# Kernel tuning notes

Measured on AMD Instinct MI355X. Metric: run time of the kernel, lower is better.

The kernel has to match this reference:

```python
import jax, jax.numpy as jnp
import numpy as np
from jax import lax

X_SIZE, Z_SIZE, H, GC, PD = 256, 64, 64, 16, 2
B, K, T = 256, 16, 50
LOG_SIG_MIN, LOG_SIG_MAX, LOG_P_MAX = -10.0, 10.0, 50.0
ZX = X_SIZE + Z_SIZE
LSTM_IN = ZX + PD


def setup_inputs() -> dict:
    key = jax.random.key(0)
    ks = jax.random.split(key, 24)
    s = lambda fan_in: 1.0 / np.sqrt(fan_in)
    u = lambda k, shape, sc: jax.random.uniform(k, shape, jnp.float32, -sc, sc)
    inp = {
        'x': jax.random.normal(ks[0], (B, X_SIZE), jnp.float32),
        'z_stacked': jax.random.normal(ks[1], (K, B, Z_SIZE), jnp.float32),
        'input_seqs': jax.random.normal(ks[2], (B, 8, 2, 2, 6), jnp.float32),
        'pred_seqs': jax.random.normal(ks[3], (B, T, 2, 2, 6), jnp.float32),
        # initial_h / initial_c linears: ZX -> H
        'Wh0': u(ks[4], (H, ZX), s(ZX)), 'bh0': u(ks[5], (H,), s(ZX)),
        'Wc0': u(ks[6], (H, ZX), s(ZX)), 'bc0': u(ks[7], (H,), s(ZX)),
        # LSTMCell: gates order i,f,g,o
        'Wih': u(ks[8], (4 * H, LSTM_IN), s(H)), 'Whh': u(ks[9], (4 * H, H), s(H)),
        'bih': u(ks[10], (4 * H,), s(H)), 'bhh': u(ks[11], (4 * H,), s(H)),
        # GMM parameter heads: H -> GC / GC*PD
        'Wpi': u(ks[12], (GC, H), s(H)), 'bpi': u(ks[13], (GC,), s(H)),
        'Wmu': u(ks[14], (GC * PD, H), s(H)), 'bmu': u(ks[15], (GC * PD,), s(H)),
        'Wls': u(ks[16], (GC * PD, H), s(H)), 'bls': u(ks[17], (GC * PD,), s(H)),
        'Wcorr': u(ks[18], (GC, H), s(H)), 'bcorr': u(ks[19], (GC,), s(H)),
        'n_z_samples': K,
    }
    return inp


def _gmm2d_log_prob(log_pis, mus, log_sigmas, corrs, value):
    # log_pis/corrs: [K,B,T,GC]; mus/log_sigmas: [K,B,T,GC*PD]; value: [B,T,PD]
    ls = jnp.clip(log_sigmas, LOG_SIG_MIN, LOG_SIG_MAX).reshape(K, B, T, GC, PD)
    mu = mus.reshape(K, B, T, GC, PD)
    dx = value[None, :, :, None, :] - mu                      # [K,B,T,GC,PD]
    zscore = dx * jnp.exp(-ls)                                # dx / sigma
    one_m_rho2 = 1.0 - corrs ** 2
    quad = (zscore[..., 0] ** 2 + zscore[..., 1] ** 2
            - 2.0 * corrs * zscore[..., 0] * zscore[..., 1])
    comp = (-jnp.log(2.0 * jnp.pi) - ls.sum(-1)
            - 0.5 * jnp.log(one_m_rho2) - 0.5 * quad / one_m_rho2)
    log_pi_n = jax.nn.log_softmax(log_pis, axis=-1)
    log_p_t = jax.nn.logsumexp(log_pi_n + comp, axis=-1)      # [K,B,T]
    return jnp.minimum(log_p_t, LOG_P_MAX)


def reference(x, z_stacked, input_seqs, pred_seqs,
              Wh0, bh0, Wc0, bc0, Wih, Whh, bih, bhh,
              Wpi, bpi, Wmu, bmu, Wls, bls, Wcorr, bcorr, n_z_samples):
    tgt_future = pred_seqs[:, :, 1, 1, 2:4]                   # [B,T,2]
    tgt_present = input_seqs[:, -1, 1, 1, 2:4]                # [B,2]
    z = z_stacked.reshape(-1, z_stacked.shape[-1])            # [K*B, z]
    zx = jnp.concatenate([z, jnp.tile(x, (n_z_samples, 1))], axis=1)  # [N, ZX]
    N = zx.shape[0]
    h0 = zx @ Wh0.T + bh0
    c0 = zx @ Wc0.T + bc0
    decode_inputs = jnp.concatenate([tgt_present[:, None, :], tgt_future[:, :T - 1, :]], axis=1)  # [B,T,2]
    inputs = jnp.concatenate([
        jnp.broadcast_to(zx[:, None, :], (N, T, ZX)),
        jnp.tile(decode_inputs, (n_z_samples, 1, 1))], axis=2)  # [N,T,ZX+2]

    def step(carry, xt):
        h, c = carry
        gates = xt @ Wih.T + bih + h @ Whh.T + bhh
        i, f, g, o = jnp.split(gates, 4, axis=-1)
        c = jax.nn.sigmoid(f) * c + jax.nn.sigmoid(i) * jnp.tanh(g)
        h = jax.nn.sigmoid(o) * jnp.tanh(c)
        return (h, c), h

    _, hs = lax.scan(step, (h0, c0), jnp.swapaxes(inputs, 0, 1))  # [T,N,H]
    hs = jnp.swapaxes(hs, 0, 1)                                   # [N,T,H]

    log_pis = (hs @ Wpi.T + bpi).reshape(K, B, T, GC)
    mus = (hs @ Wmu.T + bmu).reshape(K, B, T, GC * PD)
    log_sigmas = (hs @ Wls.T + bls).reshape(K, B, T, GC * PD)
    corrs = jnp.tanh(hs @ Wcorr.T + bcorr).reshape(K, B, T, GC)

    log_p_yt_xz = _gmm2d_log_prob(log_pis, mus, log_sigmas, corrs, tgt_future)
    return log_p_yt_xz.sum(axis=2)                                # [K,B]
```

## Files before the change

kernel.cpp:

```cpp
#include <hip/hip_runtime.h>


#define T_ 50
#define SPB 16
#define ZXS 324
#define HFS 72
#define GLS 256
#define PLS 100

typedef __attribute__((ext_vector_type(8))) short short8;
typedef __attribute__((ext_vector_type(4))) float f32x4;

#define MFMA(a, b, c) __builtin_amdgcn_mfma_f32_16x16x32_bf16(a, b, c, 0, 0, 0)

__device__ __forceinline__ float sigf(float x)  { return 1.0f / (1.0f + __expf(-x)); }
__device__ __forceinline__ float tanh_(float x) { return 1.0f - 2.0f / (__expf(2.0f * x) + 1.0f); }

__device__ __forceinline__ void splitf(float f, unsigned short& hi, unsigned short& lo) {
    unsigned b = __float_as_uint(f);
    hi = (unsigned short)(b >> 16);
    float fh = __uint_as_float(b & 0xffff0000u);
    lo = (unsigned short)(__float_as_uint(f - fh) >> 16);
}

__device__ __forceinline__ void pack8(const float* p, short8& hi, short8& lo) {
    #pragma unroll
    for (int e = 0; e < 8; ++e) {
        unsigned short h, l;
        splitf(p[e], h, l);
        hi[e] = (short)h; lo[e] = (short)l;
    }
}

__launch_bounds__(512, 2)
__global__ void decoder_kernel(
    const float* __restrict__ x,       const float* __restrict__ z,
    const float* __restrict__ inp_seqs,const float* __restrict__ pred_seqs,
    const float* __restrict__ Wh0,     const float* __restrict__ bh0,
    const float* __restrict__ Wc0,     const float* __restrict__ bc0,
    const float* __restrict__ Wih,     const float* __restrict__ Whh,
    const float* __restrict__ bih,     const float* __restrict__ bhh,
    const float* __restrict__ Wpi,     const float* __restrict__ bpi,
    const float* __restrict__ Wmu,     const float* __restrict__ bmu,
    const float* __restrict__ Wls,     const float* __restrict__ bls,
    const float* __restrict__ Wcorr,   const float* __restrict__ bcorr,
    float* __restrict__ out)
{
    __shared__ __align__(16) float smem[9504];
    float* ZXL = smem;
    float* GL  = smem;
    float* PL  = smem + 4096;
    float* C0X = smem + 5696;
    unsigned short* HFhi = (unsigned short*)(smem + 6720);
    unsigned short* HFlo = (unsigned short*)(smem + 7296);
    float* FUT = smem + 7872;
    float* PRS = smem + 9472;

    const int j = threadIdx.x;
    const int w = j >> 6;
    const int l = j & 63;
    const int g = l >> 4;
    const int c = l & 15;
    const int blk = blockIdx.x;

    for (int e = j; e < SPB*320; e += 512) {
        int s = e / 320, k = e - s*320;
        int n = blk*SPB + s; int kk = n >> 8; int b = n & 255;
        ZXL[s*ZXS + k] = (k < 64) ? z[(kk*256 + b)*64 + k] : x[b*256 + (k - 64)];
    }
    for (int e = j; e < T_*SPB; e += 512) {
        int t = e >> 4, s = e & 15;
        int b = (blk*SPB + s) & 255;
        float2 v = *reinterpret_cast<const float2*>(pred_seqs + b*1200 + t*24 + 20);
        FUT[t*32 + s*2] = v.x; FUT[t*32 + s*2 + 1] = v.y;
    }
    if (j < SPB) {
        int b = (blk*SPB + j) & 255;
        float2 v = *reinterpret_cast<const float2*>(inp_seqs + b*192 + 188);
        PRS[j*2] = v.x; PRS[j*2 + 1] = v.y;
    }
    __syncthreads();

    const int gate0 = w*32 + c;
    const int gate1 = w*32 + 16 + c;
    const int colB  = w*16 + c;

    f32x4 gc0, gc1, accB;
    {
        float bA0 = bih[gate0] + bhh[gate0];
        float bA1 = bih[gate1] + bhh[gate1];
        float bB  = (w < 4) ? bh0[colB] : bc0[colB - 64];
        gc0 = (f32x4){bA0, bA0, bA0, bA0};
        gc1 = (f32x4){bA1, bA1, bA1, bA1};
        accB = (f32x4){bB, bB, bB, bB};
    }
    const float* rowA0 = Wih + gate0*322;
    const float* rowA1 = Wih + gate1*322;
    const float* rowB  = (w < 4) ? (Wh0 + colB*320) : (Wc0 + (colB - 64)*320);

    for (int ks = 0; ks < 10; ++ks) {
        int k0 = ks*32 + g*8;
        short8 ahi, alo, b0h, b0l, b1h, b1l, bbh, bbl;
        pack8(&ZXL[c*ZXS + k0], ahi, alo);
        pack8(rowA0 + k0, b0h, b0l);
        pack8(rowA1 + k0, b1h, b1l);
        pack8(rowB  + k0, bbh, bbl);
        gc0  = MFMA(ahi, b0h, gc0);  gc0  = MFMA(ahi, b0l, gc0);  gc0  = MFMA(alo, b0h, gc0);
        gc1  = MFMA(ahi, b1h, gc1);  gc1  = MFMA(ahi, b1l, gc1);  gc1  = MFMA(alo, b1h, gc1);
        accB = MFMA(ahi, bbh, accB); accB = MFMA(ahi, bbl, accB); accB = MFMA(alo, bbh, accB);
    }

    if (w < 4) {
        #pragma unroll
        for (int r = 0; r < 4; ++r) {
            int s = g*4 + r;
            unsigned short hh, ll; splitf(accB[r], hh, ll);
            HFhi[s*HFS + colB] = hh; HFlo[s*HFS + colB] = ll;
        }
    } else {
        #pragma unroll
        for (int r = 0; r < 4; ++r) C0X[(g*4 + r)*64 + (colB - 64)] = accB[r];
    }

    const float wd00 = rowA0[320], wd01 = rowA0[321];
    const float wd10 = rowA1[320], wd11 = rowA1[321];
    short8 w1h00, w1l00, w1h01, w1l01, w1h10, w1l10, w1h11, w1l11;
    pack8(Whh + gate0*64 +      g*8, w1h00, w1l00);
    pack8(Whh + gate0*64 + 32 + g*8, w1h01, w1l01);
    pack8(Whh + gate1*64 +      g*8, w1h10, w1l10);
    pack8(Whh + gate1*64 + 32 + g*8, w1h11, w1l11);

    short8 b3h0, b3l0, b3h1, b3l1;
    float bias3;
    {
        int r3 = (w < 6) ? (w*16 + c) : 0;
        const float* prow; float bb;
        if (r3 < 16)      { prow = Wpi   + r3*64;       bb = bpi[r3]; }
        else if (r3 < 48) { prow = Wmu   + (r3-16)*64;  bb = bmu[r3-16]; }
        else if (r3 < 80) { prow = Wls   + (r3-48)*64;  bb = bls[r3-48]; }
        else              { prow = Wcorr + (r3-80)*64;  bb = bcorr[r3-80]; }
        bias3 = bb;
        pack8(prow +      g*8, b3h0, b3l0);
        pack8(prow + 32 + g*8, b3h1, b3l1);
    }

    __syncthreads();

    const int u2 = j & 63, sg2 = j >> 6;
    float cst0 = C0X[(2*sg2 + 0)*64 + u2];
    float cst1 = C0X[(2*sg2 + 1)*64 + u2];

    const int s3 = j >> 4, g3 = j & 15;
    float sum = 0.0f;

    for (int t = 0; t < T_; ++t) {
        {
            const float* dptr = (t == 0) ? PRS : &FUT[(t-1)*32];
            f32x4 a0, a1;
            #pragma unroll
            for (int r = 0; r < 4; ++r) {
                float2 dv = *reinterpret_cast<const float2*>(dptr + (g*4 + r)*2);
                a0[r] = gc0[r] + dv.x*wd00 + dv.y*wd01;
                a1[r] = gc1[r] + dv.x*wd10 + dv.y*wd11;
            }
            short8 ah0 = *reinterpret_cast<const short8*>(HFhi + c*HFS +      g*8);
            short8 al0 = *reinterpret_cast<const short8*>(HFlo + c*HFS +      g*8);
            short8 ah1 = *reinterpret_cast<const short8*>(HFhi + c*HFS + 32 + g*8);
            short8 al1 = *reinterpret_cast<const short8*>(HFlo + c*HFS + 32 + g*8);
            a0 = MFMA(ah0, w1h00, a0); a0 = MFMA(ah0, w1l00, a0); a0 = MFMA(al0, w1h00, a0);
            a0 = MFMA(ah1, w1h01, a0); a0 = MFMA(ah1, w1l01, a0); a0 = MFMA(al1, w1h01, a0);
            a1 = MFMA(ah0, w1h10, a1); a1 = MFMA(ah0, w1l10, a1); a1 = MFMA(al0, w1h10, a1);
            a1 = MFMA(ah1, w1h11, a1); a1 = MFMA(ah1, w1l11, a1); a1 = MFMA(al1, w1h11, a1);
            #pragma unroll
            for (int r = 0; r < 4; ++r) {
                GL[(g*4 + r)*GLS + gate0] = a0[r];
                GL[(g*4 + r)*GLS + gate1] = a1[r];
            }
        }
        __syncthreads();

        {
            #pragma unroll
            for (int i = 0; i < 2; ++i) {
                int s = 2*sg2 + i;
                float gi = GL[s*GLS + u2];
                float gf = GL[s*GLS + 64  + u2];
                float gg = GL[s*GLS + 128 + u2];
                float go = GL[s*GLS + 192 + u2];
                float cp = (i == 0) ? cst0 : cst1;
                float cc = sigf(gf)*cp + sigf(gi)*tanh_(gg);
                if (i == 0) cst0 = cc; else cst1 = cc;
                float hh = sigf(go)*tanh_(cc);
                unsigned short uh, ul; splitf(hh, uh, ul);
                HFhi[s*HFS + u2] = uh; HFlo[s*HFS + u2] = ul;
            }
        }
        __syncthreads();

        if (w < 6) {
            short8 ah0 = *reinterpret_cast<const short8*>(HFhi + c*HFS +      g*8);
            short8 al0 = *reinterpret_cast<const short8*>(HFlo + c*HFS +      g*8);
            short8 ah1 = *reinterpret_cast<const short8*>(HFhi + c*HFS + 32 + g*8);
            short8 al1 = *reinterpret_cast<const short8*>(HFlo + c*HFS + 32 + g*8);
            f32x4 p = (f32x4){bias3, bias3, bias3, bias3};
            p = MFMA(ah0, b3h0, p); p = MFMA(ah0, b3l0, p); p = MFMA(al0, b3h0, p);
            p = MFMA(ah1, b3h1, p); p = MFMA(ah1, b3l1, p); p = MFMA(al1, b3h1, p);
            #pragma unroll
            for (int r = 0; r < 4; ++r) PL[(g*4 + r)*PLS + w*16 + c] = p[r];
        }
        __syncthreads();

        if (j < 256) {
            const float* pls = PL + s3*PLS;
            float a_pi = pls[g3];
            float a_m0 = pls[16 + 2*g3], a_m1 = pls[17 + 2*g3];
            float l0   = pls[48 + 2*g3], l1   = pls[49 + 2*g3];
            float a_co = pls[80 + g3];
            float v0 = FUT[t*32 + s3*2], v1 = FUT[t*32 + s3*2 + 1];
            l0 = fminf(fmaxf(l0, -10.0f), 10.0f);
            l1 = fminf(fmaxf(l1, -10.0f), 10.0f);
            float z0 = (v0 - a_m0) * __expf(-l0);
            float z1 = (v1 - a_m1) * __expf(-l1);
            float ct = tanh_(a_co);
            float omr = 1.0f - ct*ct;
            float quad = z0*z0 + z1*z1 - 2.0f*ct*z0*z1;
            float comp = -1.8378770664093453f - (l0 + l1) - 0.5f*__logf(omr) - 0.5f*quad/omr;
            float a = a_pi + comp;
            float m1v = a, m2v = a_pi;
            #pragma unroll
            for (int off = 1; off < 16; off <<= 1) {
                m1v = fmaxf(m1v, __shfl_xor(m1v, off));
                m2v = fmaxf(m2v, __shfl_xor(m2v, off));
            }
            float e1 = __expf(a - m1v), e2 = __expf(a_pi - m2v);
            #pragma unroll
            for (int off = 1; off < 16; off <<= 1) {
                e1 += __shfl_xor(e1, off);
                e2 += __shfl_xor(e2, off);
            }
            float logp = (m1v + __logf(e1)) - (m2v + __logf(e2));
            sum += fminf(logp, 50.0f);
        }
    }

    if (j < 256 && g3 == 0) out[blk*SPB + s3] = sum;
}

extern "C" void kernel_launch(void* const* d_in, const int* in_sizes, int n_in,
                              void* d_out, int out_size, void* d_ws, size_t ws_size,
                              hipStream_t stream) {
    const float* x     = (const float*)d_in[0];
    const float* z     = (const float*)d_in[1];
    const float* iseq  = (const float*)d_in[2];
    const float* pseq  = (const float*)d_in[3];
    const float* Wh0   = (const float*)d_in[4];
    const float* bh0   = (const float*)d_in[5];
    const float* Wc0   = (const float*)d_in[6];
    const float* bc0   = (const float*)d_in[7];
    const float* Wih   = (const float*)d_in[8];
    const float* Whh   = (const float*)d_in[9];
    const float* bih   = (const float*)d_in[10];
    const float* bhh   = (const float*)d_in[11];
    const float* Wpi   = (const float*)d_in[12];
    const float* bpi   = (const float*)d_in[13];
    const float* Wmu   = (const float*)d_in[14];
    const float* bmu   = (const float*)d_in[15];
    const float* Wls   = (const float*)d_in[16];
    const float* bls   = (const float*)d_in[17];
    const float* Wcorr = (const float*)d_in[18];
    const float* bcorr = (const float*)d_in[19];
    float* out = (float*)d_out;

    decoder_kernel<<<256, 512, 0, stream>>>(x, z, iseq, pseq, Wh0, bh0, Wc0, bc0,
                                            Wih, Whh, bih, bhh, Wpi, bpi, Wmu, bmu,
                                            Wls, bls, Wcorr, bcorr, out);
}
```

Measured before the change: 112.7 us.

## Split decoder into weight-pack, LSTM recurrence, and parallel GMM head kernels

```diff
diff --git a/kernel.cpp b/kernel.cpp
--- a/kernel.cpp
+++ b/kernel.cpp
@@ -2,16 +2,18 @@
 
 
 #define T_ 50
-#define SPB 16
-#define ZXS 324
-#define HFS 72
-#define GLS 256
-#define PLS 100
 
 typedef __attribute__((ext_vector_type(8))) short short8;
 typedef __attribute__((ext_vector_type(4))) float f32x4;
 
 #define MFMA(a, b, c) __builtin_amdgcn_mfma_f32_16x16x32_bf16(a, b, c, 0, 0, 0)
+
+#define HBYTES 26214400
+#define WIH_B 0
+#define WH0_B 20480
+#define WC0_B 25600
+#define WHH_B 30720
+#define PRJ_B 34816
 
 __device__ __forceinline__ float sigf(float x)  { return 1.0f / (1.0f + __expf(-x)); }
 __device__ __forceinline__ float tanh_(float x) { return 1.0f - 2.0f / (__expf(2.0f * x) + 1.0f); }
@@ -32,218 +34,309 @@
     }
 }
 
-__launch_bounds__(512, 2)
-__global__ void decoder_kernel(
-    const float* __restrict__ x,       const float* __restrict__ z,
-    const float* __restrict__ inp_seqs,const float* __restrict__ pred_seqs,
-    const float* __restrict__ Wh0,     const float* __restrict__ bh0,
-    const float* __restrict__ Wc0,     const float* __restrict__ bc0,
-    const float* __restrict__ Wih,     const float* __restrict__ Whh,
-    const float* __restrict__ bih,     const float* __restrict__ bhh,
-    const float* __restrict__ Wpi,     const float* __restrict__ bpi,
-    const float* __restrict__ Wmu,     const float* __restrict__ bmu,
-    const float* __restrict__ Wls,     const float* __restrict__ bls,
-    const float* __restrict__ Wcorr,   const float* __restrict__ bcorr,
-    float* __restrict__ out)
+__global__ void pack_kernel(const float* __restrict__ Wih, const float* __restrict__ Whh,
+                            const float* __restrict__ Wh0, const float* __restrict__ Wc0,
+                            const float* __restrict__ Wpi, const float* __restrict__ Wmu,
+                            const float* __restrict__ Wls, const float* __restrict__ Wcorr,
+                            short8* __restrict__ WF)
 {
-    __shared__ __align__(16) float smem[9504];
+    int id = blockIdx.x * 256 + threadIdx.x;
+    if (id >= 18176) return;
+    const float* src;
+    int dst0, dst1;
+    if (id < 10240) {
+        int ks = id >> 10, rem = id & 1023;
+        int q = rem >> 8, rem2 = rem & 255;
+        int w = rem2 >> 6, l = rem2 & 63;
+        int g = l >> 4, c = l & 15;
+        src = Wih + (q*64 + w*16 + c)*322 + ks*32 + g*8;
+        dst0 = WIH_B + (((ks*4 + q)*2 + 0)*4 + w)*64 + l;
+        dst1 = WIH_B + (((ks*4 + q)*2 + 1)*4 + w)*64 + l;
+    } else if (id < 12800) {
+        int t2 = id - 10240;
+        int ks = t2 >> 8, rem = t2 & 255;
+        int w = rem >> 6, l = rem & 63;
+        int g = l >> 4, c = l & 15;
+        src = Wh0 + (w*16 + c)*320 + ks*32 + g*8;
+        dst0 = WH0_B + ((ks*2 + 0)*4 + w)*64 + l;
+        dst1 = WH0_B + ((ks*2 + 1)*4 + w)*64 + l;
+    } else if (id < 15360) {
+        int t2 = id - 12800;
+        int ks = t2 >> 8, rem = t2 & 255;
+        int w = rem >> 6, l = rem & 63;
+        int g = l >> 4, c = l & 15;
+        src = Wc0 + (w*16 + c)*320 + ks*32 + g*8;
+        dst0 = WC0_B + ((ks*2 + 0)*4 + w)*64 + l;
+        dst1 = WC0_B + ((ks*2 + 1)*4 + w)*64 + l;
+    } else if (id < 17408) {
+        int t3 = id - 15360;
+        int q = t3 >> 9, rem = t3 & 511;
+        int ks = rem >> 8, rem2 = rem & 255;
+        int w = rem2 >> 6, l = rem2 & 63;
+        int g = l >> 4, c = l & 15;
+        src = Whh + (q*64 + w*16 + c)*64 + ks*32 + g*8;
+        dst0 = WHH_B + (((q*2 + ks)*2 + 0)*4 + w)*64 + l;
+        dst1 = WHH_B + (((q*2 + ks)*2 + 1)*4 + w)*64 + l;
+    } else {
+        int t4 = id - 17408;
+        int pt = t4 >> 7, rem = t4 & 127;
+        int ks = rem >> 6, l = rem & 63;
+        int g = l >> 4, c = l & 15;
+        int r3 = pt*16 + c;
+        const float* p;
+        if      (r3 < 16) p = Wpi   + r3*64;
+        else if (r3 < 48) p = Wmu   + (r3-16)*64;
+        else if (r3 < 80) p = Wls   + (r3-48)*64;
+        else              p = Wcorr + (r3-80)*64;
+        src = p + ks*32 + g*8;
+        dst0 = PRJ_B + ((pt*2 + ks)*2 + 0)*64 + l;
+        dst1 = PRJ_B + ((pt*2 + ks)*2 + 1)*64 + l;
+    }
+    short8 hi, lo;
+    pack8(src, hi, lo);
+    WF[dst0] = hi;
+    WF[dst1] = lo;
+}
+
+__launch_bounds__(256, 2)
+__global__ void lstm_kernel(
+    const float* __restrict__ x,        const float* __restrict__ z,
+    const float* __restrict__ inp_seqs, const float* __restrict__ pred_seqs,
+    const float* __restrict__ Wih,      const float* __restrict__ bh0,
+    const float* __restrict__ bc0,      const float* __restrict__ bih,
+    const float* __restrict__ bhh,
+    unsigned short* __restrict__ Hout,  const short8* __restrict__ WF)
+{
+    __shared__ __align__(16) float smem[4560];
     float* ZXL = smem;
-    float* GL  = smem;
-    float* PL  = smem + 4096;
-    float* C0X = smem + 5696;
-    unsigned short* HFhi = (unsigned short*)(smem + 6720);
-    unsigned short* HFlo = (unsigned short*)(smem + 7296);
-    float* FUT = smem + 7872;
-    float* PRS = smem + 9472;
-
+    unsigned short* HB = (unsigned short*)(smem + 2592);
+    unsigned short* H0h = HB;
+    unsigned short* H0l = HB + 576;
+    unsigned short* H1h = HB + 1152;
+    unsigned short* H1l = HB + 1728;
+    float* FUT = smem + 3744;
+    float* PRS = smem + 4544;
+
+    const int j = threadIdx.x;
+    const int w = j >> 6;
+    const int l = j & 63;
+    const int g = l >> 4;
+    const int c = l & 15;
+    const int U = w*16 + c;
+    const int blk = blockIdx.x;
+
+    for (int e = j; e < 8*320; e += 256) {
+        int s = e / 320, k = e - s*320;
+        int n = blk*8 + s, kk = n >> 8, b = n & 255;
+        ZXL[s*324 + k] = (k < 64) ? z[(kk*256 + b)*64 + k] : x[b*256 + (k - 64)];
+    }
+    for (int e = j; e < T_*16; e += 256) {
+        int t = e >> 4, s = (e >> 1) & 7;
+        int b = (blk*8 + s) & 255;
+        FUT[e] = pred_seqs[b*1200 + t*24 + 20 + (e & 1)];
+    }
+    if (j < 16) {
+        int b = (blk*8 + (j >> 1)) & 255;
+        PRS[j] = inp_seqs[b*192 + 188 + (j & 1)];
+    }
+    __syncthreads();
+
+    const int R0 = U, R1 = 64+U, R2 = 128+U, R3 = 192+U;
+    f32x4 gc[4], h0a, c0a;
+    {
+        float b0 = bih[R0]+bhh[R0], b1 = bih[R1]+bhh[R1];
+        float b2 = bih[R2]+bhh[R2], b3 = bih[R3]+bhh[R3];
+        gc[0] = (f32x4){b0,b0,b0,b0}; gc[1] = (f32x4){b1,b1,b1,b1};
+        gc[2] = (f32x4){b2,b2,b2,b2}; gc[3] = (f32x4){b3,b3,b3,b3};
+        float bh_ = bh0[U], bc_ = bc0[U];
+        h0a = (f32x4){bh_,bh_,bh_,bh_};
+        c0a = (f32x4){bc_,bc_,bc_,bc_};
+    }
+    for (int ks = 0; ks < 10; ++ks) {
+        short8 ahi, alo;
+        pack8(&ZXL[(c & 7)*324 + ks*32 + g*8], ahi, alo);
+        #pragma unroll
+        for (int q = 0; q < 4; ++q) {
+            short8 Bh = WF[WIH_B + (((ks*4 + q)*2 + 0)*4 + w)*64 + l];
+            short8 Bl = WF[WIH_B + (((ks*4 + q)*2 + 1)*4 + w)*64 + l];
+            gc[q] = MFMA(ahi, Bh, gc[q]);
+            gc[q] = MFMA(ahi, Bl, gc[q]);
+            gc[q] = MFMA(alo, Bh, gc[q]);
+        }
+        {
+            short8 Bh = WF[WH0_B + ((ks*2 + 0)*4 + w)*64 + l];
+            short8 Bl = WF[WH0_B + ((ks*2 + 1)*4 + w)*64 + l];
+            h0a = MFMA(ahi, Bh, h0a); h0a = MFMA(ahi, Bl, h0a); h0a = MFMA(alo, Bh, h0a);
+        }
+        {
+            short8 Bh = WF[WC0_B + ((ks*2 + 0)*4 + w)*64 + l];
+            short8 Bl = WF[WC0_B + ((ks*2 + 1)*4 + w)*64 + l];
+            c0a = MFMA(ahi, Bh, c0a); c0a = MFMA(ahi, Bl, c0a); c0a = MFMA(alo, Bh, c0a);
+        }
+    }
+
+    const bool lowg = (g < 2);
+    const int s0 = 4*(g & 1) + (lowg ? 0 : 2);
+    float cst0 = lowg ? c0a[0] : c0a[2];
+    float cst1 = lowg ? c0a[1] : c0a[3];
+    {
+        float hv0 = lowg ? h0a[0] : h0a[2];
+        float hv1 = lowg ? h0a[1] : h0a[3];
+        unsigned short hh, ll;
+        splitf(hv0, hh, ll); H0h[s0*72 + U] = hh; H0l[s0*72 + U] = ll;
+        splitf(hv1, hh, ll); H0h[(s0+1)*72 + U] = hh; H0l[(s0+1)*72 + U] = ll;
+    }
+
+    float wd0[4], wd1[4];
+    wd0[0] = Wih[R0*322+320]; wd1[0] = Wih[R0*322+321];
+    wd0[1] = Wih[R1*322+320]; wd1[1] = Wih[R1*322+321];
+    wd0[2] = Wih[R2*322+320]; wd1[2] = Wih[R2*322+321];
+    wd0[3] = Wih[R3*322+320]; wd1[3] = Wih[R3*322+321];
+    short8 WB[4][2][2];
+    #pragma unroll
+    for (int q = 0; q < 4; ++q)
+        #pragma unroll
+        for (int ks = 0; ks < 2; ++ks)
+            #pragma unroll
+            for (int p = 0; p < 2; ++p)
+                WB[q][ks][p] = WF[WHH_B + (((q*2 + ks)*2 + p)*4 + w)*64 + l];
+
+    __syncthreads();
+
+    const int nbase = blk*8;
+    for (int t = 0; t < T_; ++t) {
+        const unsigned short* Hh = (t & 1) ? H1h : H0h;
+        const unsigned short* Hl = (t & 1) ? H1l : H0l;
+        unsigned short* Nh = (t & 1) ? H0h : H1h;
+        unsigned short* Nl = (t & 1) ? H0l : H1l;
+
+        short8 ah0 = *reinterpret_cast<const short8*>(Hh + (c & 7)*72 + g*8);
+        short8 al0 = *reinterpret_cast<const short8*>(Hl + (c & 7)*72 + g*8);
+        short8 ah1 = *reinterpret_cast<const short8*>(Hh + (c & 7)*72 + 32 + g*8);
+        short8 al1 = *reinterpret_cast<const short8*>(Hl + (c & 7)*72 + 32 + g*8);
+
+        const float* dptr = (t == 0) ? PRS : (FUT + (t-1)*16);
+        float2 dvr[4];
+        #pragma unroll
+        for (int r = 0; r < 4; ++r)
+            dvr[r] = *reinterpret_cast<const float2*>(dptr + ((4*g + r) & 7)*2);
+
+        f32x4 aq[4];
+        #pragma unroll
+        for (int q = 0; q < 4; ++q) {
+            #pragma unroll
+            for (int r = 0; r < 4; ++r)
+                aq[q][r] = gc[q][r] + dvr[r].x*wd0[q] + dvr[r].y*wd1[q];
+            aq[q] = MFMA(ah0, WB[q][0][0], aq[q]);
+            aq[q] = MFMA(ah0, WB[q][0][1], aq[q]);
+            aq[q] = MFMA(al0, WB[q][0][0], aq[q]);
+            aq[q] = MFMA(ah1, WB[q][1][0], aq[q]);
+            aq[q] = MFMA(ah1, WB[q][1][1], aq[q]);
+            aq[q] = MFMA(al1, WB[q][1][0], aq[q]);
+        }
+
+        float i0 = lowg ? aq[0][0] : aq[0][2], i1 = lowg ? aq[0][1] : aq[0][3];
+        float f0 = lowg ? aq[1][0] : aq[1][2], f1 = lowg ? aq[1][1] : aq[1][3];
+        float g0 = lowg ? aq[2][0] : aq[2][2], g1 = lowg ? aq[2][1] : aq[2][3];
+        float o0 = lowg ? aq[3][0] : aq[3][2], o1 = lowg ? aq[3][1] : aq[3][3];
+        float cc0 = sigf(f0)*cst0 + sigf(i0)*tanh_(g0); cst0 = cc0;
+        float cc1 = sigf(f1)*cst1 + sigf(i1)*tanh_(g1); cst1 = cc1;
+        float hv0 = sigf(o0)*tanh_(cc0);
+        float hv1 = sigf(o1)*tanh_(cc1);
+
+        unsigned short hh0, ll0, hh1, ll1;
+        splitf(hv0, hh0, ll0);
+        splitf(hv1, hh1, ll1);
+        Hout[(size_t)(t*4096 + nbase + s0)*64 + U]     = hh0;
+        Hout[(size_t)(t*4096 + nbase + s0 + 1)*64 + U] = hh1;
+        Nh[s0*72 + U] = hh0;  Nl[s0*72 + U] = ll0;
+        Nh[(s0+1)*72 + U] = hh1;  Nl[(s0+1)*72 + U] = ll1;
+        __syncthreads();
+    }
+}
+
+__launch_bounds__(256, 3)
+__global__ void head_kernel(const float* __restrict__ pred_seqs,
+                            const float* __restrict__ bpi, const float* __restrict__ bmu,
+                            const float* __restrict__ bls, const float* __restrict__ bcorr,
+                            const unsigned short* __restrict__ Hin,
+                            const short8* __restrict__ WF,
+                            float* __restrict__ out)
+{
+    __shared__ __align__(16) float PL[4][1600];
     const int j = threadIdx.x;
     const int w = j >> 6;
     const int l = j & 63;
     const int g = l >> 4;
     const int c = l & 15;
     const int blk = blockIdx.x;
-
-    for (int e = j; e < SPB*320; e += 512) {
-        int s = e / 320, k = e - s*320;
-        int n = blk*SPB + s; int kk = n >> 8; int b = n & 255;
-        ZXL[s*ZXS + k] = (k < 64) ? z[(kk*256 + b)*64 + k] : x[b*256 + (k - 64)];
-    }
-    for (int e = j; e < T_*SPB; e += 512) {
-        int t = e >> 4, s = e & 15;
-        int b = (blk*SPB + s) & 255;
-        float2 v = *reinterpret_cast<const float2*>(pred_seqs + b*1200 + t*24 + 20);
-        FUT[t*32 + s*2] = v.x; FUT[t*32 + s*2 + 1] = v.y;
-    }
-    if (j < SPB) {
-        int b = (blk*SPB + j) & 255;
-        float2 v = *reinterpret_cast<const float2*>(inp_seqs + b*192 + 188);
-        PRS[j*2] = v.x; PRS[j*2 + 1] = v.y;
-    }
-    __syncthreads();
-
-    const int gate0 = w*32 + c;
-    const int gate1 = w*32 + 16 + c;
-    const int colB  = w*16 + c;
-
-    f32x4 gc0, gc1, accB;
-    {
-        float bA0 = bih[gate0] + bhh[gate0];
-        float bA1 = bih[gate1] + bhh[gate1];
-        float bB  = (w < 4) ? bh0[colB] : bc0[colB - 64];
-        gc0 = (f32x4){bA0, bA0, bA0, bA0};
-        gc1 = (f32x4){bA1, bA1, bA1, bA1};
-        accB = (f32x4){bB, bB, bB, bB};
-    }
-    const float* rowA0 = Wih + gate0*322;
-    const float* rowA1 = Wih + gate1*322;
-    const float* rowB  = (w < 4) ? (Wh0 + colB*320) : (Wc0 + (colB - 64)*320);
-
-    for (int ks = 0; ks < 10; ++ks) {
-        int k0 = ks*32 + g*8;
-        short8 ahi, alo, b0h, b0l, b1h, b1l, bbh, bbl;
-        pack8(&ZXL[c*ZXS + k0], ahi, alo);
-        pack8(rowA0 + k0, b0h, b0l);
-        pack8(rowA1 + k0, b1h, b1l);
-        pack8(rowB  + k0, bbh, bbl);
-        gc0  = MFMA(ahi, b0h, gc0);  gc0  = MFMA(ahi, b0l, gc0);  gc0  = MFMA(alo, b0h, gc0);
-        gc1  = MFMA(ahi, b1h, gc1);  gc1  = MFMA(ahi, b1l, gc1);  gc1  = MFMA(alo, b1h, gc1);
-        accB = MFMA(ahi, bbh, accB); accB = MFMA(ahi, bbl, accB); accB = MFMA(alo, bbh, accB);
-    }
-
-    if (w < 4) {
-        #pragma unroll
-        for (int r = 0; r < 4; ++r) {
-            int s = g*4 + r;
-            unsigned short hh, ll; splitf(accB[r], hh, ll);
-            HFhi[s*HFS + colB] = hh; HFlo[s*HFS + colB] = ll;
-        }
-    } else {
-        #pragma unroll
-        for (int r = 0; r < 4; ++r) C0X[(g*4 + r)*64 + (colB - 64)] = accB[r];
-    }
-
-    const float wd00 = rowA0[320], wd01 = rowA0[321];
-    const float wd10 = rowA1[320], wd11 = rowA1[321];
-    short8 w1h00, w1l00, w1h01, w1l01, w1h10, w1l10, w1h11, w1l11;
-    pack8(Whh + gate0*64 +      g*8, w1h00, w1l00);
-    pack8(Whh + gate0*64 + 32 + g*8, w1h01, w1l01);
-    pack8(Whh + gate1*64 +      g*8, w1h10, w1l10);
-    pack8(Whh + gate1*64 + 32 + g*8, w1h11, w1l11);
-
-    short8 b3h0, b3l0, b3h1, b3l1;
-    float bias3;
-    {
-        int r3 = (w < 6) ? (w*16 + c) : 0;
-        const float* prow; float bb;
-        if (r3 < 16)      { prow = Wpi   + r3*64;       bb = bpi[r3]; }
-        else if (r3 < 48) { prow = Wmu   + (r3-16)*64;  bb = bmu[r3-16]; }
-        else if (r3 < 80) { prow = Wls   + (r3-48)*64;  bb = bls[r3-48]; }
-        else              { prow = Wcorr + (r3-80)*64;  bb = bcorr[r3-80]; }
-        bias3 = bb;
-        pack8(prow +      g*8, b3h0, b3l0);
-        pack8(prow + 32 + g*8, b3h1, b3l1);
-    }
-
-    __syncthreads();
-
-    const int u2 = j & 63, sg2 = j >> 6;
-    float cst0 = C0X[(2*sg2 + 0)*64 + u2];
-    float cst1 = C0X[(2*sg2 + 1)*64 + u2];
-
-    const int s3 = j >> 4, g3 = j & 15;
-    float sum = 0.0f;
-
-    for (int t = 0; t < T_; ++t) {
-        {
-            const float* dptr = (t == 0) ? PRS : &FUT[(t-1)*32];
-            f32x4 a0, a1;
+    const int set = blk >> 2, chunk = blk & 3;
+    const int t0 = (chunk*25) >> 1, t1 = ((chunk+1)*25) >> 1;
+
+    float bias[6];
+    #pragma unroll
+    for (int pt = 0; pt < 6; ++pt) {
+        int r3 = pt*16 + c;
+        bias[pt] = (r3 < 16) ? bpi[r3] : (r3 < 48) ? bmu[r3-16]
+                 : (r3 < 80) ? bls[r3-48] : bcorr[r3-80];
+    }
+
+    const int s = l >> 2, q4 = l & 3;
+    const int n_s = set*16 + s, b_s = n_s & 255;
+    float* PLw = &PL[w][0];
+    float sum_local = 0.0f;
+
+    for (int t = t0 + w; t < t1; t += 4) {
+        const unsigned short* hp = Hin + (size_t)(t*4096 + set*16 + c)*64;
+        short8 ah0 = *reinterpret_cast<const short8*>(hp + g*8);
+        short8 ah1 = *reinterpret_cast<const short8*>(hp + 32 + g*8);
+        #pragma unroll
+        for (int pt = 0; pt < 6; ++pt) {
+            short8 B00 = WF[PRJ_B + ((pt*2 + 0)*2 + 0)*64 + l];
+            short8 B01 = WF[PRJ_B + ((pt*2 + 0)*2 + 1)*64 + l];
+            short8 B10 = WF[PRJ_B + ((pt*2 + 1)*2 + 0)*64 + l];
+            short8 B11 = WF[PRJ_B + ((pt*2 + 1)*2 + 1)*64 + l];
+            f32x4 p = (f32x4){bias[pt], bias[pt], bias[pt], bias[pt]};
+            p = MFMA(ah0, B00, p);
+            p = MFMA(ah0, B01, p);
+            p = MFMA(ah1, B10, p);
+            p = MFMA(ah1, B11, p);
             #pragma unroll
-            for (int r = 0; r < 4; ++r) {
-                float2 dv = *reinterpret_cast<const float2*>(dptr + (g*4 + r)*2);
-                a0[r] = gc0[r] + dv.x*wd00 + dv.y*wd01;
-                a1[r] = gc1[r] + dv.x*wd10 + dv.y*wd11;
-            }
-            short8 ah0 = *reinterpret_cast<const short8*>(HFhi + c*HFS +      g*8);
-            short8 al0 = *reinterpret_cast<const short8*>(HFlo + c*HFS +      g*8);
-            short8 ah1 = *reinterpret_cast<const short8*>(HFhi + c*HFS + 32 + g*8);
-            short8 al1 = *reinterpret_cast<const short8*>(HFlo + c*HFS + 32 + g*8);
-            a0 = MFMA(ah0, w1h00, a0); a0 = MFMA(ah0, w1l00, a0); a0 = MFMA(al0, w1h00, a0);
-            a0 = MFMA(ah1, w1h01, a0); a0 = MFMA(ah1, w1l01, a0); a0 = MFMA(al1, w1h01, a0);
-            a1 = MFMA(ah0, w1h10, a1); a1 = MFMA(ah0, w1l10, a1); a1 = MFMA(al0, w1h10, a1);
-            a1 = MFMA(ah1, w1h11, a1); a1 = MFMA(ah1, w1l11, a1); a1 = MFMA(al1, w1h11, a1);
-            #pragma unroll
-            for (int r = 0; r < 4; ++r) {
-                GL[(g*4 + r)*GLS + gate0] = a0[r];
-                GL[(g*4 + r)*GLS + gate1] = a1[r];
-            }
-        }
-        __syncthreads();
-
-        {
-            #pragma unroll
-            for (int i = 0; i < 2; ++i) {
-                int s = 2*sg2 + i;
-                float gi = GL[s*GLS + u2];
-                float gf = GL[s*GLS + 64  + u2];
-                float gg = GL[s*GLS + 128 + u2];
-                float go = GL[s*GLS + 192 + u2];
-                float cp = (i == 0) ? cst0 : cst1;
-                float cc = sigf(gf)*cp + sigf(gi)*tanh_(gg);
-                if (i == 0) cst0 = cc; else cst1 = cc;
-                float hh = sigf(go)*tanh_(cc);
-                unsigned short uh, ul; splitf(hh, uh, ul);
-                HFhi[s*HFS + u2] = uh; HFlo[s*HFS + u2] = ul;
-            }
-        }
-        __syncthreads();
-
-        if (w < 6) {
-            short8 ah0 = *reinterpret_cast<const short8*>(HFhi + c*HFS +      g*8);
-            short8 al0 = *reinterpret_cast<const short8*>(HFlo + c*HFS +      g*8);
-            short8 ah1 = *reinterpret_cast<const short8*>(HFhi + c*HFS + 32 + g*8);
-            short8 al1 = *reinterpret_cast<const short8*>(HFlo + c*HFS + 32 + g*8);
-            f32x4 p = (f32x4){bias3, bias3, bias3, bias3};
-            p = MFMA(ah0, b3h0, p); p = MFMA(ah0, b3l0, p); p = MFMA(al0, b3h0, p);
-            p = MFMA(ah1, b3h1, p); p = MFMA(ah1, b3l1, p); p = MFMA(al1, b3h1, p);
-            #pragma unroll
-            for (int r = 0; r < 4; ++r) PL[(g*4 + r)*PLS + w*16 + c] = p[r];
-        }
-        __syncthreads();
-
-        if (j < 256) {
-            const float* pls = PL + s3*PLS;
-            float a_pi = pls[g3];
-            float a_m0 = pls[16 + 2*g3], a_m1 = pls[17 + 2*g3];
-            float l0   = pls[48 + 2*g3], l1   = pls[49 + 2*g3];
-            float a_co = pls[80 + g3];
-            float v0 = FUT[t*32 + s3*2], v1 = FUT[t*32 + s3*2 + 1];
-            l0 = fminf(fmaxf(l0, -10.0f), 10.0f);
-            l1 = fminf(fmaxf(l1, -10.0f), 10.0f);
-            float z0 = (v0 - a_m0) * __expf(-l0);
-            float z1 = (v1 - a_m1) * __expf(-l1);
-            float ct = tanh_(a_co);
+            for (int r = 0; r < 4; ++r) PLw[(4*g + r)*100 + pt*16 + c] = p[r];
+        }
+        asm volatile("s_waitcnt lgkmcnt(0)" ::: "memory");
+        __builtin_amdgcn_sched_barrier(0);
+
+        float2 tv = *reinterpret_cast<const float2*>(pred_seqs + b_s*1200 + t*24 + 20);
+        float a[4], m = -1e30f, Ppi = 0.0f;
+        #pragma unroll
+        for (int i = 0; i < 4; ++i) {
+            int cq = q4*4 + i;
+            float pi = PLw[s*100 + cq];
+            float2 mu = *reinterpret_cast<const float2*>(PLw + s*100 + 16 + 2*cq);
+            float2 ls = *reinterpret_cast<const float2*>(PLw + s*100 + 48 + 2*cq);
+            float co = PLw[s*100 + 80 + cq];
+            float l0 = fminf(fmaxf(ls.x, -10.0f), 10.0f);
+            float l1 = fminf(fmaxf(ls.y, -10.0f), 10.0f);
+            float z0 = (tv.x - mu.x) * __expf(-l0);
+            float z1 = (tv.y - mu.y) * __expf(-l1);
+            float ct = tanh_(co);
             float omr = 1.0f - ct*ct;
             float quad = z0*z0 + z1*z1 - 2.0f*ct*z0*z1;
             float comp = -1.8378770664093453f - (l0 + l1) - 0.5f*__logf(omr) - 0.5f*quad/omr;
-            float a = a_pi + comp;
-            float m1v = a, m2v = a_pi;
-            #pragma unroll
-            for (int off = 1; off < 16; off <<= 1) {
-                m1v = fmaxf(m1v, __shfl_xor(m1v, off));
-                m2v = fmaxf(m2v, __shfl_xor(m2v, off));
-            }
-            float e1 = __expf(a - m1v), e2 = __expf(a_pi - m2v);
-            #pragma unroll
-            for (int off = 1; off < 16; off <<= 1) {
-                e1 += __shfl_xor(e1, off);
-                e2 += __shfl_xor(e2, off);
-            }
-            float logp = (m1v + __logf(e1)) - (m2v + __logf(e2));
-            sum += fminf(logp, 50.0f);
-        }
-    }
-
-    if (j < 256 && g3 == 0) out[blk*SPB + s3] = sum;
+            a[i] = pi + comp;
+            m = fmaxf(m, a[i]);
+            Ppi += __expf(pi);
+        }
+        m = fmaxf(m, __shfl_xor(m, 1));
+        m = fmaxf(m, __shfl_xor(m, 2));
+        float E = __expf(a[0]-m) + __expf(a[1]-m) + __expf(a[2]-m) + __expf(a[3]-m);
+        E   += __shfl_xor(E, 1);   E   += __shfl_xor(E, 2);
+        Ppi += __shfl_xor(Ppi, 1); Ppi += __shfl_xor(Ppi, 2);
+        float logp = m + __logf(E) - __logf(Ppi);
+        sum_local += fminf(logp, 50.0f);
+    }
+    if (q4 == 0) atomicAdd(out + n_s, sum_local);
 }
 
 extern "C" void kernel_launch(void* const* d_in, const int* in_sizes, int n_in,
@@ -271,7 +364,14 @@
     const float* bcorr = (const float*)d_in[19];
     float* out = (float*)d_out;
 
-    decoder_kernel<<<256, 512, 0, stream>>>(x, z, iseq, pseq, Wh0, bh0, Wc0, bc0,
-                                            Wih, Whh, bih, bhh, Wpi, bpi, Wmu, bmu,
-                                            Wls, bls, Wcorr, bcorr, out);
-}
+    unsigned short* Hbuf = (unsigned short*)d_ws;
+    short8* WF = (short8*)((char*)d_ws + HBYTES);
+
+    pack_kernel<<<71, 256, 0, stream>>>(Wih, Whh, Wh0, Wc0, Wpi, Wmu, Wls, Wcorr, WF);
+    lstm_kernel<<<512, 256, 0, stream>>>(x, z, iseq, pseq, Wih, bh0, bc0, bih, bhh,
+                                         Hbuf, (const short8*)WF);
+    hipMemsetAsync(d_out, 0, 4096 * sizeof(float), stream);
+    head_kernel<<<1024, 256, 0, stream>>>(pseq, bpi, bmu, bls, bcorr,
+                                          (const unsigned short*)Hbuf,
+                                          (const short8*)WF, out);
+}
```

After: 114.6 us. No clear change (+1.6%).
